# Performance work log

Hardware: AMD Instinct MI355X
Metric: run time of the kernel (lower is better)

The kernel has to match this reference:

```python
import jax, jax.numpy as jnp
import numpy as np

N = 50000   # nodes
E = 800000  # edges (avg degree 16)
F = 256     # in_feats
H = 4       # num_heads
D = 64      # out_feats per head (H*D == F)


def setup_inputs() -> dict:
    key = jax.random.key(0)
    ks = jax.random.split(key, 10)
    s = 0.02
    HD = H * D
    return {
        "feat": jax.random.normal(ks[0], (N, F), jnp.float32),
        "src": jax.random.randint(ks[1], (E,), 0, N),
        "dst": jax.random.randint(ks[2], (E,), 0, N),
        "Wq": jax.random.normal(ks[3], (HD, F), jnp.float32) * s,
        "bq": jnp.zeros((HD,), jnp.float32),
        "Wk": jax.random.normal(ks[4], (HD, F), jnp.float32) * s,
        "bk": jnp.zeros((HD,), jnp.float32),
        "Wv": jax.random.normal(ks[5], (HD, F), jnp.float32) * s,
        "bv": jnp.zeros((HD,), jnp.float32),
        "Wskip": jax.random.normal(ks[6], (HD, F), jnp.float32) * s,
        "bskip": jnp.zeros((HD,), jnp.float32),
        "Wgate": jax.random.normal(ks[7], (1, 3 * HD), jnp.float32) * s,
        "bgate": jnp.zeros((1,), jnp.float32),
        "ln_w": jnp.ones((HD,), jnp.float32),
        "ln_b": jnp.zeros((HD,), jnp.float32),
        "prelu_a": jnp.float32(0.25),
    }


def reference(feat, src, dst, Wq, bq, Wk, bk, Wv, bv, Wskip, bskip,
              Wgate, bgate, ln_w, ln_b, prelu_a):
    n = feat.shape[0]
    scale = 1.0 / np.sqrt(D).astype(np.float32)
    # projections: note DGL code names q from src nodes, k from dst nodes
    q = (feat @ Wq.T + bq).reshape(n, H, D)
    k = (feat @ Wk.T + bk).reshape(n, H, D)
    v = (feat @ Wv.T + bv).reshape(n, H, D)
    # per-edge scores: u_dot_v('ft','ft') = q[src] . k[dst], scaled
    e = jnp.einsum('ehd,ehd->eh', q[src], k[dst]) * scale  # [E, H]
    # edge softmax over incoming edges of each destination node
    m = jax.ops.segment_max(e, dst, num_segments=n)          # [N, H]
    ex = jnp.exp(e - m[dst])
    denom = jax.ops.segment_sum(ex, dst, num_segments=n)    # [N, H]
    sa = ex / denom[dst]                                     # [E, H]
    # weighted scatter-aggregate: sum_e sa * v[src]
    agg = jax.ops.segment_sum(sa[:, :, None] * v[src], dst, num_segments=n)
    rst = agg.reshape(n, H * D)
    # gated skip connection
    skip = feat @ Wskip.T + bskip
    g = jax.nn.sigmoid(
        jnp.concatenate([skip, rst, skip - rst], axis=-1) @ Wgate.T + bgate)
    rst = g * skip + (1.0 - g) * rst
    # layer norm
    mu = rst.mean(-1, keepdims=True)
    var = rst.var(-1, keepdims=True)
    rst = (rst - mu) * jax.lax.rsqrt(var + 1e-5) * ln_w + ln_b
    # PReLU
    return jnp.where(rst >= 0, rst, prelu_a * rst)
```

## Files before the change

### kernel.cpp

```cpp
#include <hip/hip_runtime.h>
#include <math.h>


typedef __attribute__((ext_vector_type(8))) short short8;
typedef __attribute__((ext_vector_type(4))) float floatx4;
typedef __attribute__((ext_vector_type(2))) float floatx2;
typedef __attribute__((address_space(3))) void lds_void;
typedef __attribute__((address_space(1))) const void gbl_void;

__device__ inline unsigned short f2bf(float x) {
    unsigned int u = __float_as_uint(x);
    u = (u + 0x7fffu + ((u >> 16) & 1u)) >> 16;
    return (unsigned short)u;
}
__device__ inline float bf2f(unsigned short u) {
    return __uint_as_float(((unsigned int)u) << 16);
}

__global__ void prep_kernel(const float* __restrict__ f, ushort* __restrict__ fb,
                            int n_elems, int total_pad,
                            const float* __restrict__ Wq, const float* __restrict__ Wk,
                            const float* __restrict__ Wv, const float* __restrict__ Wsk,
                            const float* __restrict__ bq, const float* __restrict__ bk,
                            const float* __restrict__ bv, const float* __restrict__ bsk,
                            const float* __restrict__ Wg,
                            ushort* __restrict__ Wcat, float* __restrict__ bcat,
                            float* __restrict__ wgs, float* __restrict__ wgr,
                            int* __restrict__ counts, int* __restrict__ cursor, int n)
{
    int g = blockIdx.x * blockDim.x + threadIdx.x;
    int featQ = total_pad >> 2;
    if (g < featQ) {
        int i = g * 4;
        float4 v = (i < n_elems) ? *(const float4*)(f + i) : make_float4(0.f, 0.f, 0.f, 0.f);
        ushort4 u;
        u.x = f2bf(v.x); u.y = f2bf(v.y); u.z = f2bf(v.z); u.w = f2bf(v.w);
        *(ushort4*)(fb + i) = u;
        return;
    }
    int g2 = g - featQ;
    if (g2 < 65536) {
        int i = g2 * 4;
        int mat = i >> 16;
        int rem = i & 65535;
        const float* W = (mat == 0) ? Wq : (mat == 1) ? Wk : (mat == 2) ? Wv : Wsk;
        float4 v = *(const float4*)(W + rem);
        ushort4 u;
        u.x = f2bf(v.x); u.y = f2bf(v.y); u.z = f2bf(v.z); u.w = f2bf(v.w);
        *(ushort4*)(Wcat + i) = u;
        return;
    }
    int g3 = g2 - 65536;
    if (g3 < 256) {
        int o = g3 * 4;
        int mat = o >> 8;
        const float* b = (mat == 0) ? bq : (mat == 1) ? bk : (mat == 2) ? bv : bsk;
        *(float4*)(bcat + o) = *(const float4*)(b + (o & 255));
        return;
    }
    int g4 = g3 - 256;
    if (g4 < 64) {
        int o = g4 * 4;
        float4 a = *(const float4*)(Wg + o);
        float4 c = *(const float4*)(Wg + 512 + o);
        *(float4*)(wgs + o) = make_float4(a.x + c.x, a.y + c.y, a.z + c.z, a.w + c.w);
        return;
    }
    if (g4 < 128) {
        int o = (g4 - 64) * 4;
        float4 b = *(const float4*)(Wg + 256 + o);
        float4 c = *(const float4*)(Wg + 512 + o);
        *(float4*)(wgr + o) = make_float4(b.x - c.x, b.y - c.y, b.z - c.z, b.w - c.w);
        return;
    }
    int g5 = g4 - 128;
    if (g5 < n) counts[g5] = 0;
    if (g5 == 0) *cursor = 0;
}


__global__ void count_kernel(const int* __restrict__ dst, int* counts, int e) {
    int i = blockIdx.x * blockDim.x + threadIdx.x;
    if (i < e) atomicAdd(&counts[dst[i]], 1);
}

__global__ void alloc_kernel(const int* __restrict__ counts, int* start, int* cur,
                             int* cursor, int n) {
    int i = blockIdx.x * blockDim.x + threadIdx.x;
    int lane = threadIdx.x & 63;
    int c = (i < n) ? counts[i] : 0;
    int incl = c;
#pragma unroll
    for (int d = 1; d < 64; d <<= 1) {
        int t = __shfl_up(incl, d);
        if (lane >= d) incl += t;
    }
    int waveTot = __shfl(incl, 63);
    int base = 0;
    if (lane == 63) base = atomicAdd(cursor, waveTot);
    base = __shfl(base, 63);
    if (i < n) {
        int s = base + incl - c;
        start[i] = s;
        cur[i] = s;
    }
}

__global__ void fill_kernel(const int* __restrict__ dst, const int* __restrict__ src,
                            int* cur, int* srclist, int e) {
    int i = blockIdx.x * blockDim.x + threadIdx.x;
    if (i < e) {
        int pos = atomicAdd(&cur[dst[i]], 1);
        srclist[pos] = src[i];
    }
}

__global__ __launch_bounds__(512) void mfma_gemm(
    const ushort* __restrict__ featb, const ushort* __restrict__ Wcat,
    const float* __restrict__ bcat,
    unsigned char* __restrict__ qv8, ushort* __restrict__ kb,
    ushort* __restrict__ sb, int n)
{
    __shared__ ushort At[128 * 32];
    __shared__ ushort Bt[256 * 32];
    int tid = threadIdx.x;
    int lane = tid & 63;
    int wv = tid >> 6;
    int ysel = blockIdx.x;
    int mBase = blockIdx.y * 128;
    int nBlk = ysel * 256;
    int mQuad = (wv & 1) * 64;
    int nQuad = (wv >> 1) * 64;

    floatx4 zero = {0.f, 0.f, 0.f, 0.f};
    floatx4 acc[4][4];
#pragma unroll
    for (int i = 0; i < 4; ++i)
#pragma unroll
        for (int j = 0; j < 4; ++j) acc[i][j] = zero;

    int rsel = lane & 15;
    int ksel = (lane >> 4) * 8;
    int lrow = lane >> 2;
    int lcol = (lane & 3) * 8;

    for (int k0 = 0; k0 < 256; k0 += 32) {
        {
            int row = 16 * wv + lrow;
            const ushort* gp = featb + (size_t)(mBase + row) * 256 + k0 + lcol;
            __builtin_amdgcn_global_load_lds((gbl_void*)gp, (lds_void*)&At[16 * wv * 32], 16, 0, 0);
        }
#pragma unroll
        for (int r = 0; r < 2; ++r) {
            int row = 32 * wv + 16 * r + lrow;
            const ushort* gp = Wcat + (size_t)(nBlk + row) * 256 + k0 + lcol;
            __builtin_amdgcn_global_load_lds((gbl_void*)gp, (lds_void*)&Bt[(32 * wv + 16 * r) * 32], 16, 0, 0);
        }
        __syncthreads();
        short8 af[4], bf[4];
#pragma unroll
        for (int i = 0; i < 4; ++i)
            af[i] = *(const short8*)&At[(mQuad + 16 * i + rsel) * 32 + ksel];
#pragma unroll
        for (int j = 0; j < 4; ++j)
            bf[j] = *(const short8*)&Bt[(nQuad + 16 * j + rsel) * 32 + ksel];
#pragma unroll
        for (int i = 0; i < 4; ++i)
#pragma unroll
            for (int j = 0; j < 4; ++j)
                acc[i][j] = __builtin_amdgcn_mfma_f32_16x16x32_bf16(bf[j], af[i], acc[i][j], 0, 0, 0);
        __syncthreads();
    }

    int rowq4 = (lane >> 4) * 4;
    float4 bias[4];
#pragma unroll
    for (int nt = 0; nt < 4; ++nt)
        bias[nt] = *(const float4*)(bcat + nBlk + nQuad + 16 * nt + rowq4);

    if (ysel == 0 || ysel == 2) {
        unsigned char* outp = qv8 + ((ysel == 0) ? 0 : 256);
#pragma unroll
        for (int mt = 0; mt < 4; ++mt) {
            int m = mBase + mQuad + 16 * mt + (lane & 15);
            if (m < n) {
                unsigned char* rowp = outp + (size_t)m * 512 + nQuad + rowq4;
#pragma unroll
                for (int nt = 0; nt < 4; ++nt) {
                    int pk = __builtin_amdgcn_cvt_pk_fp8_f32(
                        acc[mt][nt][0] + bias[nt].x, acc[mt][nt][1] + bias[nt].y, 0, false);
                    pk = __builtin_amdgcn_cvt_pk_fp8_f32(
                        acc[mt][nt][2] + bias[nt].z, acc[mt][nt][3] + bias[nt].w, pk, true);
                    *(int*)(rowp + 16 * nt) = pk;
                }
            }
        }
    } else {
        ushort* outp = (ysel == 1) ? kb : sb;
#pragma unroll
        for (int mt = 0; mt < 4; ++mt) {
            int m = mBase + mQuad + 16 * mt + (lane & 15);
            if (m < n) {
                ushort* rowp = outp + (size_t)m * 256 + nQuad + rowq4;
#pragma unroll
                for (int nt = 0; nt < 4; ++nt) {
                    uint lo = (uint)f2bf(acc[mt][nt][0] + bias[nt].x)
                            | ((uint)f2bf(acc[mt][nt][1] + bias[nt].y) << 16);
                    uint hi = (uint)f2bf(acc[mt][nt][2] + bias[nt].z)
                            | ((uint)f2bf(acc[mt][nt][3] + bias[nt].w) << 16);
                    *(uint2*)(rowp + 16 * nt) = make_uint2(lo, hi);
                }
            }
        }
    }
}

__global__ __launch_bounds__(256) void node_kernel(
    const unsigned char* __restrict__ qv8, const ushort* __restrict__ kb,
    const ushort* __restrict__ sbuf,
    const int* __restrict__ srclist, const int* __restrict__ start,
    const int* __restrict__ counts,
    const float* __restrict__ wgs, const float* __restrict__ wgr,
    const float* __restrict__ bg,
    const float* __restrict__ lnw, const float* __restrict__ lnb,
    const float* __restrict__ pa,
    float* __restrict__ out, int n, int E)
{
    int wvi = threadIdx.x >> 6;
    int lane = threadIdx.x & 63;
    int node = blockIdx.x * 4 + wvi;
    if (node >= n) return;

    int l32 = lane & 31;
    int half = lane >> 5;
    int f0 = l32 * 8;

    short8 kv = *(const short8*)(kb + (size_t)node * 256 + f0);
    float kf[8];
#pragma unroll
    for (int i = 0; i < 8; ++i) kf[i] = bf2f((unsigned short)kv[i]);

    float acc[8];
#pragma unroll
    for (int i = 0; i < 8; ++i) acc[i] = 0.f;
    float denom = 0.f;

    int sidx = start[node], cnt = counts[node];

    for (int base = 0; base < cnt; base += 64) {
        int m = min(64, cnt - base);
        int batch = srclist[min(sidx + base + lane, E - 1)];
        for (int j = 0; j < m; j += 8) {
            int e0 = j + half;
            int e1 = e0 + 2;
            int e2 = e0 + 4;
            int e3 = e0 + 6;
            bool vld0 = e0 < m;
            bool vld1 = e1 < m;
            bool vld2 = e2 < m;
            bool vld3 = e3 < m;
            int s0 = __shfl(batch, vld0 ? e0 : 0);
            int s1 = __shfl(batch, vld1 ? e1 : 0);
            int s2 = __shfl(batch, vld2 ? e2 : 0);
            int s3 = __shfl(batch, vld3 ? e3 : 0);
            const unsigned char* p0 = qv8 + (size_t)s0 * 512 + f0;
            const unsigned char* p1 = qv8 + (size_t)s1 * 512 + f0;
            const unsigned char* p2 = qv8 + (size_t)s2 * 512 + f0;
            const unsigned char* p3 = qv8 + (size_t)s3 * 512 + f0;
            uint2 qw0 = *(const uint2*)p0;
            uint2 qw1 = *(const uint2*)p1;
            uint2 qw2 = *(const uint2*)p2;
            uint2 qw3 = *(const uint2*)p3;
            uint2 vw0 = *(const uint2*)(p0 + 256);
            uint2 vw1 = *(const uint2*)(p1 + 256);
            uint2 vw2 = *(const uint2*)(p2 + 256);
            uint2 vw3 = *(const uint2*)(p3 + 256);

            floatx2 a0l = __builtin_amdgcn_cvt_pk_f32_fp8(qw0.x, false);
            floatx2 a0h = __builtin_amdgcn_cvt_pk_f32_fp8(qw0.x, true);
            floatx2 a0m = __builtin_amdgcn_cvt_pk_f32_fp8(qw0.y, false);
            floatx2 a0t = __builtin_amdgcn_cvt_pk_f32_fp8(qw0.y, true);
            floatx2 a1l = __builtin_amdgcn_cvt_pk_f32_fp8(qw1.x, false);
            floatx2 a1h = __builtin_amdgcn_cvt_pk_f32_fp8(qw1.x, true);
            floatx2 a1m = __builtin_amdgcn_cvt_pk_f32_fp8(qw1.y, false);
            floatx2 a1t = __builtin_amdgcn_cvt_pk_f32_fp8(qw1.y, true);
            floatx2 a2l = __builtin_amdgcn_cvt_pk_f32_fp8(qw2.x, false);
            floatx2 a2h = __builtin_amdgcn_cvt_pk_f32_fp8(qw2.x, true);
            floatx2 a2m = __builtin_amdgcn_cvt_pk_f32_fp8(qw2.y, false);
            floatx2 a2t = __builtin_amdgcn_cvt_pk_f32_fp8(qw2.y, true);
            floatx2 a3l = __builtin_amdgcn_cvt_pk_f32_fp8(qw3.x, false);
            floatx2 a3h = __builtin_amdgcn_cvt_pk_f32_fp8(qw3.x, true);
            floatx2 a3m = __builtin_amdgcn_cvt_pk_f32_fp8(qw3.y, false);
            floatx2 a3t = __builtin_amdgcn_cvt_pk_f32_fp8(qw3.y, true);

            float p0f = a0l[0]*kf[0]; p0f = fmaf(a0l[1], kf[1], p0f);
            p0f = fmaf(a0h[0], kf[2], p0f); p0f = fmaf(a0h[1], kf[3], p0f);
            p0f = fmaf(a0m[0], kf[4], p0f); p0f = fmaf(a0m[1], kf[5], p0f);
            p0f = fmaf(a0t[0], kf[6], p0f); p0f = fmaf(a0t[1], kf[7], p0f);
            float p1f = a1l[0]*kf[0]; p1f = fmaf(a1l[1], kf[1], p1f);
            p1f = fmaf(a1h[0], kf[2], p1f); p1f = fmaf(a1h[1], kf[3], p1f);
            p1f = fmaf(a1m[0], kf[4], p1f); p1f = fmaf(a1m[1], kf[5], p1f);
            p1f = fmaf(a1t[0], kf[6], p1f); p1f = fmaf(a1t[1], kf[7], p1f);
            float p2f = a2l[0]*kf[0]; p2f = fmaf(a2l[1], kf[1], p2f);
            p2f = fmaf(a2h[0], kf[2], p2f); p2f = fmaf(a2h[1], kf[3], p2f);
            p2f = fmaf(a2m[0], kf[4], p2f); p2f = fmaf(a2m[1], kf[5], p2f);
            p2f = fmaf(a2t[0], kf[6], p2f); p2f = fmaf(a2t[1], kf[7], p2f);
            float p3f = a3l[0]*kf[0]; p3f = fmaf(a3l[1], kf[1], p3f);
            p3f = fmaf(a3h[0], kf[2], p3f); p3f = fmaf(a3h[1], kf[3], p3f);
            p3f = fmaf(a3m[0], kf[4], p3f); p3f = fmaf(a3m[1], kf[5], p3f);
            p3f = fmaf(a3t[0], kf[6], p3f); p3f = fmaf(a3t[1], kf[7], p3f);

            p0f += __shfl_xor(p0f, 1);  p1f += __shfl_xor(p1f, 1);
            p2f += __shfl_xor(p2f, 1);  p3f += __shfl_xor(p3f, 1);
            p0f += __shfl_xor(p0f, 2);  p1f += __shfl_xor(p1f, 2);
            p2f += __shfl_xor(p2f, 2);  p3f += __shfl_xor(p3f, 2);
            p0f += __shfl_xor(p0f, 4);  p1f += __shfl_xor(p1f, 4);
            p2f += __shfl_xor(p2f, 4);  p3f += __shfl_xor(p3f, 4);
            float w0 = vld0 ? __expf(p0f * 0.125f) : 0.f;
            float w1 = vld1 ? __expf(p1f * 0.125f) : 0.f;
            float w2 = vld2 ? __expf(p2f * 0.125f) : 0.f;
            float w3 = vld3 ? __expf(p3f * 0.125f) : 0.f;
            denom += (w0 + w1) + (w2 + w3);

            floatx2 x0l = __builtin_amdgcn_cvt_pk_f32_fp8(vw0.x, false);
            floatx2 x0h = __builtin_amdgcn_cvt_pk_f32_fp8(vw0.x, true);
            floatx2 x0m = __builtin_amdgcn_cvt_pk_f32_fp8(vw0.y, false);
            floatx2 x0t = __builtin_amdgcn_cvt_pk_f32_fp8(vw0.y, true);
            floatx2 x1l = __builtin_amdgcn_cvt_pk_f32_fp8(vw1.x, false);
            floatx2 x1h = __builtin_amdgcn_cvt_pk_f32_fp8(vw1.x, true);
            floatx2 x1m = __builtin_amdgcn_cvt_pk_f32_fp8(vw1.y, false);
            floatx2 x1t = __builtin_amdgcn_cvt_pk_f32_fp8(vw1.y, true);
            floatx2 x2l = __builtin_amdgcn_cvt_pk_f32_fp8(vw2.x, false);
            floatx2 x2h = __builtin_amdgcn_cvt_pk_f32_fp8(vw2.x, true);
            floatx2 x2m = __builtin_amdgcn_cvt_pk_f32_fp8(vw2.y, false);
            floatx2 x2t = __builtin_amdgcn_cvt_pk_f32_fp8(vw2.y, true);
            floatx2 x3l = __builtin_amdgcn_cvt_pk_f32_fp8(vw3.x, false);
            floatx2 x3h = __builtin_amdgcn_cvt_pk_f32_fp8(vw3.x, true);
            floatx2 x3m = __builtin_amdgcn_cvt_pk_f32_fp8(vw3.y, false);
            floatx2 x3t = __builtin_amdgcn_cvt_pk_f32_fp8(vw3.y, true);

            acc[0] = fmaf(w0, x0l[0], fmaf(w1, x1l[0], fmaf(w2, x2l[0], fmaf(w3, x3l[0], acc[0]))));
            acc[1] = fmaf(w0, x0l[1], fmaf(w1, x1l[1], fmaf(w2, x2l[1], fmaf(w3, x3l[1], acc[1]))));
            acc[2] = fmaf(w0, x0h[0], fmaf(w1, x1h[0], fmaf(w2, x2h[0], fmaf(w3, x3h[0], acc[2]))));
            acc[3] = fmaf(w0, x0h[1], fmaf(w1, x1h[1], fmaf(w2, x2h[1], fmaf(w3, x3h[1], acc[3]))));
            acc[4] = fmaf(w0, x0m[0], fmaf(w1, x1m[0], fmaf(w2, x2m[0], fmaf(w3, x3m[0], acc[4]))));
            acc[5] = fmaf(w0, x0m[1], fmaf(w1, x1m[1], fmaf(w2, x2m[1], fmaf(w3, x3m[1], acc[5]))));
            acc[6] = fmaf(w0, x0t[0], fmaf(w1, x1t[0], fmaf(w2, x2t[0], fmaf(w3, x3t[0], acc[6]))));
            acc[7] = fmaf(w0, x0t[1], fmaf(w1, x1t[1], fmaf(w2, x2t[1], fmaf(w3, x3t[1], acc[7]))));
        }
    }

#pragma unroll
    for (int i = 0; i < 8; ++i) acc[i] += __shfl_xor(acc[i], 32);
    denom += __shfl_xor(denom, 32);
    float inv = (denom > 0.f) ? 1.f / denom : 0.f;
    float r[8];
#pragma unroll
    for (int i = 0; i < 8; ++i) r[i] = acc[i] * inv;

    short8 sv = *(const short8*)(sbuf + (size_t)node * 256 + f0);
    float s[8];
#pragma unroll
    for (int i = 0; i < 8; ++i) s[i] = bf2f((unsigned short)sv[i]);

    float4 g0 = *(const float4*)(wgs + f0);
    float4 g1 = *(const float4*)(wgs + f0 + 4);
    float4 h0 = *(const float4*)(wgr + f0);
    float4 h1 = *(const float4*)(wgr + f0 + 4);
    float z = g0.x*s[0] + g0.y*s[1] + g0.z*s[2] + g0.w*s[3]
            + g1.x*s[4] + g1.y*s[5] + g1.z*s[6] + g1.w*s[7]
            + h0.x*r[0] + h0.y*r[1] + h0.z*r[2] + h0.w*r[3]
            + h1.x*r[4] + h1.y*r[5] + h1.z*r[6] + h1.w*r[7];
#pragma unroll
    for (int d = 16; d >= 1; d >>= 1) z += __shfl_xor(z, d);
    z += bg[0];
    float g = 1.f / (1.f + __expf(-z));

    float y[8];
#pragma unroll
    for (int i = 0; i < 8; ++i) y[i] = g * s[i] + (1.f - g) * r[i];

    float sum = y[0]+y[1]+y[2]+y[3]+y[4]+y[5]+y[6]+y[7];
#pragma unroll
    for (int d = 16; d >= 1; d >>= 1) sum += __shfl_xor(sum, d);
    float mu = sum * (1.f / 256.f);
    float dv[8];
    float sq = 0.f;
#pragma unroll
    for (int i = 0; i < 8; ++i) { dv[i] = y[i] - mu; sq = fmaf(dv[i], dv[i], sq); }
#pragma unroll
    for (int d = 16; d >= 1; d >>= 1) sq += __shfl_xor(sq, d);
    float rstd = rsqrtf(sq * (1.f / 256.f) + 1e-5f);

    float4 lw0 = *(const float4*)(lnw + f0);
    float4 lw1 = *(const float4*)(lnw + f0 + 4);
    float4 lb0 = *(const float4*)(lnb + f0);
    float4 lb1 = *(const float4*)(lnb + f0 + 4);
    float lwv[8] = {lw0.x, lw0.y, lw0.z, lw0.w, lw1.x, lw1.y, lw1.z, lw1.w};
    float lbv[8] = {lb0.x, lb0.y, lb0.z, lb0.w, lb1.x, lb1.y, lb1.z, lb1.w};
    float ap = pa[0];
    float o[8];
#pragma unroll
    for (int i = 0; i < 8; ++i) {
        float t = dv[i] * rstd * lwv[i] + lbv[i];
        o[i] = (t >= 0.f) ? t : ap * t;
    }

    float4 stv;
    stv.x = half ? o[4] : o[0];
    stv.y = half ? o[5] : o[1];
    stv.z = half ? o[6] : o[2];
    stv.w = half ? o[7] : o[3];
    *(float4*)(out + (size_t)node * 256 + f0 + 4 * half) = stv;
}


extern "C" void kernel_launch(void* const* d_in, const int* in_sizes, int n_in,
                              void* d_out, int out_size, void* d_ws, size_t ws_size,
                              hipStream_t stream)
{
    const float* feat = (const float*)d_in[0];
    const int* src    = (const int*)d_in[1];
    const int* dst    = (const int*)d_in[2];
    const float* Wq   = (const float*)d_in[3];
    const float* bq   = (const float*)d_in[4];
    const float* Wk   = (const float*)d_in[5];
    const float* bk   = (const float*)d_in[6];
    const float* Wv   = (const float*)d_in[7];
    const float* bv   = (const float*)d_in[8];
    const float* Wsk  = (const float*)d_in[9];
    const float* bsk  = (const float*)d_in[10];
    const float* Wg   = (const float*)d_in[11];
    const float* bg   = (const float*)d_in[12];
    const float* lnw  = (const float*)d_in[13];
    const float* lnb  = (const float*)d_in[14];
    const float* pa   = (const float*)d_in[15];

    int N = in_sizes[0] / 256;
    int E = in_sizes[1];
    float* out = (float*)d_out;

    int Mtiles = (N + 127) / 128;
    int Npad = Mtiles * 128;

    char* ws = (char*)d_ws;
    size_t off = 0;
    auto alloc = [&](size_t bytes) { char* p = ws + off; off = (off + bytes + 255) & ~(size_t)255; return p; };
    ushort* featb      = (ushort*)alloc((size_t)Npad * 256 * 2);
    ushort* Wcat       = (ushort*)alloc(1024 * 256 * 2);
    float*  bcat       = (float*) alloc(1024 * 4);
    float*  wgs        = (float*) alloc(256 * 4);
    float*  wgr        = (float*) alloc(256 * 4);
    unsigned char* qv8 = (unsigned char*)alloc((size_t)N * 512);
    ushort* kb         = (ushort*)alloc((size_t)N * 256 * 2);
    ushort* sb         = (ushort*)alloc((size_t)N * 256 * 2);
    int* counts        = (int*)alloc((size_t)N * 4);
    int* startv        = (int*)alloc((size_t)N * 4);
    int* cur           = (int*)alloc((size_t)N * 4);
    int* cursor        = (int*)alloc(4);
    int* srclist       = (int*)alloc((size_t)E * 4);

    int totPad = Npad * 256;
    int prepThreads = totPad / 4 + 65536 + 256 + 128 + N;
    prep_kernel<<<(prepThreads + 255) / 256, 256, 0, stream>>>(
        feat, featb, N * 256, totPad, Wq, Wk, Wv, Wsk, bq, bk, bv, bsk, Wg,
        Wcat, bcat, wgs, wgr, counts, cursor, N);

    count_kernel<<<(E + 255) / 256, 256, 0, stream>>>(dst, counts, E);
    alloc_kernel<<<(N + 255) / 256, 256, 0, stream>>>(counts, startv, cur, cursor, N);
    fill_kernel<<<(E + 255) / 256, 256, 0, stream>>>(dst, src, cur, srclist, E);

    dim3 gg(4, Mtiles);
    mfma_gemm<<<gg, 512, 0, stream>>>(featb, Wcat, bcat, qv8, kb, sb, N);

    node_kernel<<<(N + 3) / 4, 256, 0, stream>>>(qv8, kb, sb, srclist, startv, counts,
                                                 wgs, wgr, bg, lnw, lnb, pa, out, N, E);
}
```

Baseline: 353.5 us.

## Make node kernel persistent with atomic work tickets and fuse edge counting into prep

The node aggregation kernel now launches a fixed number of waves that repeatedly grab the next destination node from a global atomic ticket, hoisting constant parameter loads out of the per-node loop. This aims to balance uneven per-node edge counts and reduce block launch overhead. Edge-degree counting is merged into the prep kernel, with counters zeroed by async memsets, removing a separate kernel launch. It adds one atomic per node and extra memset operations.

```diff
diff --git a/kernel.cpp b/kernel.cpp
--- a/kernel.cpp
+++ b/kernel.cpp
@@ -1,6 +1,8 @@
 #include <hip/hip_runtime.h>
 #include <math.h>
 
+
+#define NODE_WAVES 8192
 
 typedef __attribute__((ext_vector_type(8))) short short8;
 typedef __attribute__((ext_vector_type(4))) float floatx4;
@@ -26,9 +28,11 @@
                             const float* __restrict__ Wg,
                             ushort* __restrict__ Wcat, float* __restrict__ bcat,
                             float* __restrict__ wgs, float* __restrict__ wgr,
-                            int* __restrict__ counts, int* __restrict__ cursor, int n)
+                            int* __restrict__ counts, int* __restrict__ cursor,
+                            const int* __restrict__ dst, int e)
 {
     int g = blockIdx.x * blockDim.x + threadIdx.x;
+    if (g == 0) cursor[1] = NODE_WAVES;
     int featQ = total_pad >> 2;
     if (g < featQ) {
         int i = g * 4;
@@ -74,15 +78,9 @@
         return;
     }
     int g5 = g4 - 128;
-    if (g5 < n) counts[g5] = 0;
-    if (g5 == 0) *cursor = 0;
-}
-
-
-__global__ void count_kernel(const int* __restrict__ dst, int* counts, int e) {
-    int i = blockIdx.x * blockDim.x + threadIdx.x;
-    if (i < e) atomicAdd(&counts[dst[i]], 1);
-}
+    if (g5 < e) atomicAdd(&counts[dst[g5]], 1);
+}
+
 
 __global__ void alloc_kernel(const int* __restrict__ counts, int* start, int* cur,
                              int* cursor, int n) {
@@ -224,194 +222,201 @@
     const float* __restrict__ bg,
     const float* __restrict__ lnw, const float* __restrict__ lnb,
     const float* __restrict__ pa,
+    int* __restrict__ ticket,
     float* __restrict__ out, int n, int E)
 {
-    int wvi = threadIdx.x >> 6;
     int lane = threadIdx.x & 63;
-    int node = blockIdx.x * 4 + wvi;
-    if (node >= n) return;
-
     int l32 = lane & 31;
     int half = lane >> 5;
     int f0 = l32 * 8;
-
-    short8 kv = *(const short8*)(kb + (size_t)node * 256 + f0);
-    float kf[8];
-#pragma unroll
-    for (int i = 0; i < 8; ++i) kf[i] = bf2f((unsigned short)kv[i]);
-
-    float acc[8];
-#pragma unroll
-    for (int i = 0; i < 8; ++i) acc[i] = 0.f;
-    float denom = 0.f;
-
-    int sidx = start[node], cnt = counts[node];
-
-    for (int base = 0; base < cnt; base += 64) {
-        int m = min(64, cnt - base);
-        int batch = srclist[min(sidx + base + lane, E - 1)];
-        for (int j = 0; j < m; j += 8) {
-            int e0 = j + half;
-            int e1 = e0 + 2;
-            int e2 = e0 + 4;
-            int e3 = e0 + 6;
-            bool vld0 = e0 < m;
-            bool vld1 = e1 < m;
-            bool vld2 = e2 < m;
-            bool vld3 = e3 < m;
-            int s0 = __shfl(batch, vld0 ? e0 : 0);
-            int s1 = __shfl(batch, vld1 ? e1 : 0);
-            int s2 = __shfl(batch, vld2 ? e2 : 0);
-            int s3 = __shfl(batch, vld3 ? e3 : 0);
-            const unsigned char* p0 = qv8 + (size_t)s0 * 512 + f0;
-            const unsigned char* p1 = qv8 + (size_t)s1 * 512 + f0;
-            const unsigned char* p2 = qv8 + (size_t)s2 * 512 + f0;
-            const unsigned char* p3 = qv8 + (size_t)s3 * 512 + f0;
-            uint2 qw0 = *(const uint2*)p0;
-            uint2 qw1 = *(const uint2*)p1;
-            uint2 qw2 = *(const uint2*)p2;
-            uint2 qw3 = *(const uint2*)p3;
-            uint2 vw0 = *(const uint2*)(p0 + 256);
-            uint2 vw1 = *(const uint2*)(p1 + 256);
-            uint2 vw2 = *(const uint2*)(p2 + 256);
-            uint2 vw3 = *(const uint2*)(p3 + 256);
-
-            floatx2 a0l = __builtin_amdgcn_cvt_pk_f32_fp8(qw0.x, false);
-            floatx2 a0h = __builtin_amdgcn_cvt_pk_f32_fp8(qw0.x, true);
-            floatx2 a0m = __builtin_amdgcn_cvt_pk_f32_fp8(qw0.y, false);
-            floatx2 a0t = __builtin_amdgcn_cvt_pk_f32_fp8(qw0.y, true);
-            floatx2 a1l = __builtin_amdgcn_cvt_pk_f32_fp8(qw1.x, false);
-            floatx2 a1h = __builtin_amdgcn_cvt_pk_f32_fp8(qw1.x, true);
-            floatx2 a1m = __builtin_amdgcn_cvt_pk_f32_fp8(qw1.y, false);
-            floatx2 a1t = __builtin_amdgcn_cvt_pk_f32_fp8(qw1.y, true);
-            floatx2 a2l = __builtin_amdgcn_cvt_pk_f32_fp8(qw2.x, false);
-            floatx2 a2h = __builtin_amdgcn_cvt_pk_f32_fp8(qw2.x, true);
-            floatx2 a2m = __builtin_amdgcn_cvt_pk_f32_fp8(qw2.y, false);
-            floatx2 a2t = __builtin_amdgcn_cvt_pk_f32_fp8(qw2.y, true);
-            floatx2 a3l = __builtin_amdgcn_cvt_pk_f32_fp8(qw3.x, false);
-            floatx2 a3h = __builtin_amdgcn_cvt_pk_f32_fp8(qw3.x, true);
-            floatx2 a3m = __builtin_amdgcn_cvt_pk_f32_fp8(qw3.y, false);
-            floatx2 a3t = __builtin_amdgcn_cvt_pk_f32_fp8(qw3.y, true);
-
-            float p0f = a0l[0]*kf[0]; p0f = fmaf(a0l[1], kf[1], p0f);
-            p0f = fmaf(a0h[0], kf[2], p0f); p0f = fmaf(a0h[1], kf[3], p0f);
-            p0f = fmaf(a0m[0], kf[4], p0f); p0f = fmaf(a0m[1], kf[5], p0f);
-            p0f = fmaf(a0t[0], kf[6], p0f); p0f = fmaf(a0t[1], kf[7], p0f);
-            float p1f = a1l[0]*kf[0]; p1f = fmaf(a1l[1], kf[1], p1f);
-            p1f = fmaf(a1h[0], kf[2], p1f); p1f = fmaf(a1h[1], kf[3], p1f);
-            p1f = fmaf(a1m[0], kf[4], p1f); p1f = fmaf(a1m[1], kf[5], p1f);
-            p1f = fmaf(a1t[0], kf[6], p1f); p1f = fmaf(a1t[1], kf[7], p1f);
-            float p2f = a2l[0]*kf[0]; p2f = fmaf(a2l[1], kf[1], p2f);
-            p2f = fmaf(a2h[0], kf[2], p2f); p2f = fmaf(a2h[1], kf[3], p2f);
-            p2f = fmaf(a2m[0], kf[4], p2f); p2f = fmaf(a2m[1], kf[5], p2f);
-            p2f = fmaf(a2t[0], kf[6], p2f); p2f = fmaf(a2t[1], kf[7], p2f);
-            float p3f = a3l[0]*kf[0]; p3f = fmaf(a3l[1], kf[1], p3f);
-            p3f = fmaf(a3h[0], kf[2], p3f); p3f = fmaf(a3h[1], kf[3], p3f);
-            p3f = fmaf(a3m[0], kf[4], p3f); p3f = fmaf(a3m[1], kf[5], p3f);
-            p3f = fmaf(a3t[0], kf[6], p3f); p3f = fmaf(a3t[1], kf[7], p3f);
-
-            p0f += __shfl_xor(p0f, 1);  p1f += __shfl_xor(p1f, 1);
-            p2f += __shfl_xor(p2f, 1);  p3f += __shfl_xor(p3f, 1);
-            p0f += __shfl_xor(p0f, 2);  p1f += __shfl_xor(p1f, 2);
-            p2f += __shfl_xor(p2f, 2);  p3f += __shfl_xor(p3f, 2);
-            p0f += __shfl_xor(p0f, 4);  p1f += __shfl_xor(p1f, 4);
-            p2f += __shfl_xor(p2f, 4);  p3f += __shfl_xor(p3f, 4);
-            float w0 = vld0 ? __expf(p0f * 0.125f) : 0.f;
-            float w1 = vld1 ? __expf(p1f * 0.125f) : 0.f;
-            float w2 = vld2 ? __expf(p2f * 0.125f) : 0.f;
-            float w3 = vld3 ? __expf(p3f * 0.125f) : 0.f;
-            denom += (w0 + w1) + (w2 + w3);
-
-            floatx2 x0l = __builtin_amdgcn_cvt_pk_f32_fp8(vw0.x, false);
-            floatx2 x0h = __builtin_amdgcn_cvt_pk_f32_fp8(vw0.x, true);
-            floatx2 x0m = __builtin_amdgcn_cvt_pk_f32_fp8(vw0.y, false);
-            floatx2 x0t = __builtin_amdgcn_cvt_pk_f32_fp8(vw0.y, true);
-            floatx2 x1l = __builtin_amdgcn_cvt_pk_f32_fp8(vw1.x, false);
-            floatx2 x1h = __builtin_amdgcn_cvt_pk_f32_fp8(vw1.x, true);
-            floatx2 x1m = __builtin_amdgcn_cvt_pk_f32_fp8(vw1.y, false);
-            floatx2 x1t = __builtin_amdgcn_cvt_pk_f32_fp8(vw1.y, true);
-            floatx2 x2l = __builtin_amdgcn_cvt_pk_f32_fp8(vw2.x, false);
-            floatx2 x2h = __builtin_amdgcn_cvt_pk_f32_fp8(vw2.x, true);
-            floatx2 x2m = __builtin_amdgcn_cvt_pk_f32_fp8(vw2.y, false);
-            floatx2 x2t = __builtin_amdgcn_cvt_pk_f32_fp8(vw2.y, true);
-            floatx2 x3l = __builtin_amdgcn_cvt_pk_f32_fp8(vw3.x, false);
-            floatx2 x3h = __builtin_amdgcn_cvt_pk_f32_fp8(vw3.x, true);
-            floatx2 x3m = __builtin_amdgcn_cvt_pk_f32_fp8(vw3.y, false);
-            floatx2 x3t = __builtin_amdgcn_cvt_pk_f32_fp8(vw3.y, true);
-
-            acc[0] = fmaf(w0, x0l[0], fmaf(w1, x1l[0], fmaf(w2, x2l[0], fmaf(w3, x3l[0], acc[0]))));
-            acc[1] = fmaf(w0, x0l[1], fmaf(w1, x1l[1], fmaf(w2, x2l[1], fmaf(w3, x3l[1], acc[1]))));
-            acc[2] = fmaf(w0, x0h[0], fmaf(w1, x1h[0], fmaf(w2, x2h[0], fmaf(w3, x3h[0], acc[2]))));
-            acc[3] = fmaf(w0, x0h[1], fmaf(w1, x1h[1], fmaf(w2, x2h[1], fmaf(w3, x3h[1], acc[3]))));
-            acc[4] = fmaf(w0, x0m[0], fmaf(w1, x1m[0], fmaf(w2, x2m[0], fmaf(w3, x3m[0], acc[4]))));
-            acc[5] = fmaf(w0, x0m[1], fmaf(w1, x1m[1], fmaf(w2, x2m[1], fmaf(w3, x3m[1], acc[5]))));
-            acc[6] = fmaf(w0, x0t[0], fmaf(w1, x1t[0], fmaf(w2, x2t[0], fmaf(w3, x3t[0], acc[6]))));
-            acc[7] = fmaf(w0, x0t[1], fmaf(w1, x1t[1], fmaf(w2, x2t[1], fmaf(w3, x3t[1], acc[7]))));
-        }
-    }
-
-#pragma unroll
-    for (int i = 0; i < 8; ++i) acc[i] += __shfl_xor(acc[i], 32);
-    denom += __shfl_xor(denom, 32);
-    float inv = (denom > 0.f) ? 1.f / denom : 0.f;
-    float r[8];
-#pragma unroll
-    for (int i = 0; i < 8; ++i) r[i] = acc[i] * inv;
-
-    short8 sv = *(const short8*)(sbuf + (size_t)node * 256 + f0);
-    float s[8];
-#pragma unroll
-    for (int i = 0; i < 8; ++i) s[i] = bf2f((unsigned short)sv[i]);
 
     float4 g0 = *(const float4*)(wgs + f0);
     float4 g1 = *(const float4*)(wgs + f0 + 4);
     float4 h0 = *(const float4*)(wgr + f0);
     float4 h1 = *(const float4*)(wgr + f0 + 4);
-    float z = g0.x*s[0] + g0.y*s[1] + g0.z*s[2] + g0.w*s[3]
-            + g1.x*s[4] + g1.y*s[5] + g1.z*s[6] + g1.w*s[7]
-            + h0.x*r[0] + h0.y*r[1] + h0.z*r[2] + h0.w*r[3]
-            + h1.x*r[4] + h1.y*r[5] + h1.z*r[6] + h1.w*r[7];
-#pragma unroll
-    for (int d = 16; d >= 1; d >>= 1) z += __shfl_xor(z, d);
-    z += bg[0];
-    float g = 1.f / (1.f + __expf(-z));
-
-    float y[8];
-#pragma unroll
-    for (int i = 0; i < 8; ++i) y[i] = g * s[i] + (1.f - g) * r[i];
-
-    float sum = y[0]+y[1]+y[2]+y[3]+y[4]+y[5]+y[6]+y[7];
-#pragma unroll
-    for (int d = 16; d >= 1; d >>= 1) sum += __shfl_xor(sum, d);
-    float mu = sum * (1.f / 256.f);
-    float dv[8];
-    float sq = 0.f;
-#pragma unroll
-    for (int i = 0; i < 8; ++i) { dv[i] = y[i] - mu; sq = fmaf(dv[i], dv[i], sq); }
-#pragma unroll
-    for (int d = 16; d >= 1; d >>= 1) sq += __shfl_xor(sq, d);
-    float rstd = rsqrtf(sq * (1.f / 256.f) + 1e-5f);
-
     float4 lw0 = *(const float4*)(lnw + f0);
     float4 lw1 = *(const float4*)(lnw + f0 + 4);
     float4 lb0 = *(const float4*)(lnb + f0);
     float4 lb1 = *(const float4*)(lnb + f0 + 4);
-    float lwv[8] = {lw0.x, lw0.y, lw0.z, lw0.w, lw1.x, lw1.y, lw1.z, lw1.w};
-    float lbv[8] = {lb0.x, lb0.y, lb0.z, lb0.w, lb1.x, lb1.y, lb1.z, lb1.w};
     float ap = pa[0];
-    float o[8];
-#pragma unroll
-    for (int i = 0; i < 8; ++i) {
-        float t = dv[i] * rstd * lwv[i] + lbv[i];
-        o[i] = (t >= 0.f) ? t : ap * t;
-    }
-
-    float4 stv;
-    stv.x = half ? o[4] : o[0];
-    stv.y = half ? o[5] : o[1];
-    stv.z = half ? o[6] : o[2];
-    stv.w = half ? o[7] : o[3];
-    *(float4*)(out + (size_t)node * 256 + f0 + 4 * half) = stv;
+    float bgv = bg[0];
+
+    int node = blockIdx.x * 4 + (threadIdx.x >> 6);
+
+    while (node < n) {
+        short8 kv = *(const short8*)(kb + (size_t)node * 256 + f0);
+        float kf[8];
+#pragma unroll
+        for (int i = 0; i < 8; ++i) kf[i] = bf2f((unsigned short)kv[i]);
+
+        float acc[8];
+#pragma unroll
+        for (int i = 0; i < 8; ++i) acc[i] = 0.f;
+        float denom = 0.f;
+
+        int sidx = start[node], cnt = counts[node];
+
+        for (int base = 0; base < cnt; base += 64) {
+            int m = min(64, cnt - base);
+            int batch = srclist[min(sidx + base + lane, E - 1)];
+            for (int j = 0; j < m; j += 8) {
+                int e0 = j + half;
+                int e1 = e0 + 2;
+                int e2 = e0 + 4;
+                int e3 = e0 + 6;
+                bool vld0 = e0 < m;
+                bool vld1 = e1 < m;
+                bool vld2 = e2 < m;
+                bool vld3 = e3 < m;
+                int s0 = __shfl(batch, vld0 ? e0 : 0);
+                int s1 = __shfl(batch, vld1 ? e1 : 0);
+                int s2 = __shfl(batch, vld2 ? e2 : 0);
+                int s3 = __shfl(batch, vld3 ? e3 : 0);
+                const unsigned char* p0 = qv8 + (size_t)s0 * 512 + f0;
+                const unsigned char* p1 = qv8 + (size_t)s1 * 512 + f0;
+                const unsigned char* p2 = qv8 + (size_t)s2 * 512 + f0;
+                const unsigned char* p3 = qv8 + (size_t)s3 * 512 + f0;
+                uint2 qw0 = *(const uint2*)p0;
+                uint2 qw1 = *(const uint2*)p1;
+                uint2 qw2 = *(const uint2*)p2;
+                uint2 qw3 = *(const uint2*)p3;
+                uint2 vw0 = *(const uint2*)(p0 + 256);
+                uint2 vw1 = *(const uint2*)(p1 + 256);
+                uint2 vw2 = *(const uint2*)(p2 + 256);
+                uint2 vw3 = *(const uint2*)(p3 + 256);
+
+                floatx2 a0l = __builtin_amdgcn_cvt_pk_f32_fp8(qw0.x, false);
+                floatx2 a0h = __builtin_amdgcn_cvt_pk_f32_fp8(qw0.x, true);
+                floatx2 a0m = __builtin_amdgcn_cvt_pk_f32_fp8(qw0.y, false);
+                floatx2 a0t = __builtin_amdgcn_cvt_pk_f32_fp8(qw0.y, true);
+                floatx2 a1l = __builtin_amdgcn_cvt_pk_f32_fp8(qw1.x, false);
+                floatx2 a1h = __builtin_amdgcn_cvt_pk_f32_fp8(qw1.x, true);
+                floatx2 a1m = __builtin_amdgcn_cvt_pk_f32_fp8(qw1.y, false);
+                floatx2 a1t = __builtin_amdgcn_cvt_pk_f32_fp8(qw1.y, true);
+                floatx2 a2l = __builtin_amdgcn_cvt_pk_f32_fp8(qw2.x, false);
+                floatx2 a2h = __builtin_amdgcn_cvt_pk_f32_fp8(qw2.x, true);
+                floatx2 a2m = __builtin_amdgcn_cvt_pk_f32_fp8(qw2.y, false);
+                floatx2 a2t = __builtin_amdgcn_cvt_pk_f32_fp8(qw2.y, true);
+                floatx2 a3l = __builtin_amdgcn_cvt_pk_f32_fp8(qw3.x, false);
+                floatx2 a3h = __builtin_amdgcn_cvt_pk_f32_fp8(qw3.x, true);
+                floatx2 a3m = __builtin_amdgcn_cvt_pk_f32_fp8(qw3.y, false);
+                floatx2 a3t = __builtin_amdgcn_cvt_pk_f32_fp8(qw3.y, true);
+
+                float p0f = a0l[0]*kf[0]; p0f = fmaf(a0l[1], kf[1], p0f);
+                p0f = fmaf(a0h[0], kf[2], p0f); p0f = fmaf(a0h[1], kf[3], p0f);
+                p0f = fmaf(a0m[0], kf[4], p0f); p0f = fmaf(a0m[1], kf[5], p0f);
+                p0f = fmaf(a0t[0], kf[6], p0f); p0f = fmaf(a0t[1], kf[7], p0f);
+                float p1f = a1l[0]*kf[0]; p1f = fmaf(a1l[1], kf[1], p1f);
+                p1f = fmaf(a1h[0], kf[2], p1f); p1f = fmaf(a1h[1], kf[3], p1f);
+                p1f = fmaf(a1m[0], kf[4], p1f); p1f = fmaf(a1m[1], kf[5], p1f);
+                p1f = fmaf(a1t[0], kf[6], p1f); p1f = fmaf(a1t[1], kf[7], p1f);
+                float p2f = a2l[0]*kf[0]; p2f = fmaf(a2l[1], kf[1], p2f);
+                p2f = fmaf(a2h[0], kf[2], p2f); p2f = fmaf(a2h[1], kf[3], p2f);
+                p2f = fmaf(a2m[0], kf[4], p2f); p2f = fmaf(a2m[1], kf[5], p2f);
+                p2f = fmaf(a2t[0], kf[6], p2f); p2f = fmaf(a2t[1], kf[7], p2f);
+                float p3f = a3l[0]*kf[0]; p3f = fmaf(a3l[1], kf[1], p3f);
+                p3f = fmaf(a3h[0], kf[2], p3f); p3f = fmaf(a3h[1], kf[3], p3f);
+                p3f = fmaf(a3m[0], kf[4], p3f); p3f = fmaf(a3m[1], kf[5], p3f);
+                p3f = fmaf(a3t[0], kf[6], p3f); p3f = fmaf(a3t[1], kf[7], p3f);
+
+                p0f += __shfl_xor(p0f, 1);  p1f += __shfl_xor(p1f, 1);
+                p2f += __shfl_xor(p2f, 1);  p3f += __shfl_xor(p3f, 1);
+                p0f += __shfl_xor(p0f, 2);  p1f += __shfl_xor(p1f, 2);
+                p2f += __shfl_xor(p2f, 2);  p3f += __shfl_xor(p3f, 2);
+                p0f += __shfl_xor(p0f, 4);  p1f += __shfl_xor(p1f, 4);
+                p2f += __shfl_xor(p2f, 4);  p3f += __shfl_xor(p3f, 4);
+                float w0 = vld0 ? __expf(p0f * 0.125f) : 0.f;
+                float w1 = vld1 ? __expf(p1f * 0.125f) : 0.f;
+                float w2 = vld2 ? __expf(p2f * 0.125f) : 0.f;
+                float w3 = vld3 ? __expf(p3f * 0.125f) : 0.f;
+                denom += (w0 + w1) + (w2 + w3);
+
+                floatx2 x0l = __builtin_amdgcn_cvt_pk_f32_fp8(vw0.x, false);
+                floatx2 x0h = __builtin_amdgcn_cvt_pk_f32_fp8(vw0.x, true);
+                floatx2 x0m = __builtin_amdgcn_cvt_pk_f32_fp8(vw0.y, false);
+                floatx2 x0t = __builtin_amdgcn_cvt_pk_f32_fp8(vw0.y, true);
+                floatx2 x1l = __builtin_amdgcn_cvt_pk_f32_fp8(vw1.x, false);
+                floatx2 x1h = __builtin_amdgcn_cvt_pk_f32_fp8(vw1.x, true);
+                floatx2 x1m = __builtin_amdgcn_cvt_pk_f32_fp8(vw1.y, false);
+                floatx2 x1t = __builtin_amdgcn_cvt_pk_f32_fp8(vw1.y, true);
+                floatx2 x2l = __builtin_amdgcn_cvt_pk_f32_fp8(vw2.x, false);
+                floatx2 x2h = __builtin_amdgcn_cvt_pk_f32_fp8(vw2.x, true);
+                floatx2 x2m = __builtin_amdgcn_cvt_pk_f32_fp8(vw2.y, false);
+                floatx2 x2t = __builtin_amdgcn_cvt_pk_f32_fp8(vw2.y, true);
+                floatx2 x3l = __builtin_amdgcn_cvt_pk_f32_fp8(vw3.x, false);
+                floatx2 x3h = __builtin_amdgcn_cvt_pk_f32_fp8(vw3.x, true);
+                floatx2 x3m = __builtin_amdgcn_cvt_pk_f32_fp8(vw3.y, false);
+                floatx2 x3t = __builtin_amdgcn_cvt_pk_f32_fp8(vw3.y, true);
+
+                acc[0] = fmaf(w0, x0l[0], fmaf(w1, x1l[0], fmaf(w2, x2l[0], fmaf(w3, x3l[0], acc[0]))));
+                acc[1] = fmaf(w0, x0l[1], fmaf(w1, x1l[1], fmaf(w2, x2l[1], fmaf(w3, x3l[1], acc[1]))));
+                acc[2] = fmaf(w0, x0h[0], fmaf(w1, x1h[0], fmaf(w2, x2h[0], fmaf(w3, x3h[0], acc[2]))));
+                acc[3] = fmaf(w0, x0h[1], fmaf(w1, x1h[1], fmaf(w2, x2h[1], fmaf(w3, x3h[1], acc[3]))));
+                acc[4] = fmaf(w0, x0m[0], fmaf(w1, x1m[0], fmaf(w2, x2m[0], fmaf(w3, x3m[0], acc[4]))));
+                acc[5] = fmaf(w0, x0m[1], fmaf(w1, x1m[1], fmaf(w2, x2m[1], fmaf(w3, x3m[1], acc[5]))));
+                acc[6] = fmaf(w0, x0t[0], fmaf(w1, x1t[0], fmaf(w2, x2t[0], fmaf(w3, x3t[0], acc[6]))));
+                acc[7] = fmaf(w0, x0t[1], fmaf(w1, x1t[1], fmaf(w2, x2t[1], fmaf(w3, x3t[1], acc[7]))));
+            }
+        }
+
+#pragma unroll
+        for (int i = 0; i < 8; ++i) acc[i] += __shfl_xor(acc[i], 32);
+        denom += __shfl_xor(denom, 32);
+        float inv = (denom > 0.f) ? 1.f / denom : 0.f;
+        float r[8];
+#pragma unroll
+        for (int i = 0; i < 8; ++i) r[i] = acc[i] * inv;
+
+        short8 sv = *(const short8*)(sbuf + (size_t)node * 256 + f0);
+        float s[8];
+#pragma unroll
+        for (int i = 0; i < 8; ++i) s[i] = bf2f((unsigned short)sv[i]);
+
+        float z = g0.x*s[0] + g0.y*s[1] + g0.z*s[2] + g0.w*s[3]
+                + g1.x*s[4] + g1.y*s[5] + g1.z*s[6] + g1.w*s[7]
+                + h0.x*r[0] + h0.y*r[1] + h0.z*r[2] + h0.w*r[3]
+                + h1.x*r[4] + h1.y*r[5] + h1.z*r[6] + h1.w*r[7];
+#pragma unroll
+        for (int d = 16; d >= 1; d >>= 1) z += __shfl_xor(z, d);
+        z += bgv;
+        float g = 1.f / (1.f + __expf(-z));
+
+        float y[8];
+#pragma unroll
+        for (int i = 0; i < 8; ++i) y[i] = g * s[i] + (1.f - g) * r[i];
+
+        float sum = y[0]+y[1]+y[2]+y[3]+y[4]+y[5]+y[6]+y[7];
+#pragma unroll
+        for (int d = 16; d >= 1; d >>= 1) sum += __shfl_xor(sum, d);
+        float mu = sum * (1.f / 256.f);
+        float dv[8];
+        float sq = 0.f;
+#pragma unroll
+        for (int i = 0; i < 8; ++i) { dv[i] = y[i] - mu; sq = fmaf(dv[i], dv[i], sq); }
+#pragma unroll
+        for (int d = 16; d >= 1; d >>= 1) sq += __shfl_xor(sq, d);
+        float rstd = rsqrtf(sq * (1.f / 256.f) + 1e-5f);
+
+        float lwv[8] = {lw0.x, lw0.y, lw0.z, lw0.w, lw1.x, lw1.y, lw1.z, lw1.w};
+        float lbv[8] = {lb0.x, lb0.y, lb0.z, lb0.w, lb1.x, lb1.y, lb1.z, lb1.w};
+        float o[8];
+#pragma unroll
+        for (int i = 0; i < 8; ++i) {
+            float t = dv[i] * rstd * lwv[i] + lbv[i];
+            o[i] = (t >= 0.f) ? t : ap * t;
+        }
+
+        float4 stv;
+        stv.x = half ? o[4] : o[0];
+        stv.y = half ? o[5] : o[1];
+        stv.z = half ? o[6] : o[2];
+        stv.w = half ? o[7] : o[3];
+        *(float4*)(out + (size_t)node * 256 + f0 + 4 * half) = stv;
+
+        int t;
+        if (lane == 0) t = atomicAdd(ticket, 1);
+        node = __shfl(t, 0);
+    }
 }
 
 
@@ -457,22 +462,25 @@
     int* counts        = (int*)alloc((size_t)N * 4);
     int* startv        = (int*)alloc((size_t)N * 4);
     int* cur           = (int*)alloc((size_t)N * 4);
-    int* cursor        = (int*)alloc(4);
+    int* cursor        = (int*)alloc(8);
     int* srclist       = (int*)alloc((size_t)E * 4);
 
+    hipMemsetAsync(counts, 0, (size_t)N * 4, stream);
+    hipMemsetAsync(cursor, 0, 8, stream);
+
     int totPad = Npad * 256;
-    int prepThreads = totPad / 4 + 65536 + 256 + 128 + N;
+    int prepThreads = totPad / 4 + 65536 + 256 + 128 + E;
     prep_kernel<<<(prepThreads + 255) / 256, 256, 0, stream>>>(
         feat, featb, N * 256, totPad, Wq, Wk, Wv, Wsk, bq, bk, bv, bsk, Wg,
-        Wcat, bcat, wgs, wgr, counts, cursor, N);
-
-    count_kernel<<<(E + 255) / 256, 256, 0, stream>>>(dst, counts, E);
+        Wcat, bcat, wgs, wgr, counts, cursor, dst, E);
+
     alloc_kernel<<<(N + 255) / 256, 256, 0, stream>>>(counts, startv, cur, cursor, N);
     fill_kernel<<<(E + 255) / 256, 256, 0, stream>>>(dst, src, cur, srclist, E);
 
     dim3 gg(4, Mtiles);
     mfma_gemm<<<gg, 512, 0, stream>>>(featb, Wcat, bcat, qv8, kb, sb, N);
 
-    node_kernel<<<(N + 3) / 4, 256, 0, stream>>>(qv8, kb, sb, srclist, startv, counts,
-                                                 wgs, wgr, bg, lnw, lnb, pa, out, N, E);
-}
+    node_kernel<<<NODE_WAVES / 4, 256, 0, stream>>>(qv8, kb, sb, srclist, startv, counts,
+                                                    wgs, wgr, bg, lnw, lnb, pa,
+                                                    cursor + 1, out, N, E);
+}
```

New measurement: 872.9 us. 2.47x slower.
